# Kernel tuning notes

Hardware: AMD Instinct MI355X
Metric: run time of the kernel (lower is better)

The kernel has to match this reference:

```python
import jax, jax.numpy as jnp
import numpy as np

N = 50000        # nodes
E = 800000       # edges
D_IN = 128       # input feature dim
HID = 64         # hidden_dim
HEADS = 4
OUT = 2          # output_dim (fraud / not-fraud)
BN_EPS = 1e-5
NEG_SLOPE = 0.2  # PyG GATv2Conv default


def setup_inputs() -> dict:
    key = jax.random.key(0)
    ks = jax.random.split(key, 16)
    g = lambda k, shape, s=0.05: (jax.random.normal(k, shape, jnp.float32) * s)
    HC = HEADS * HID  # 256
    return {
        "x": jax.random.normal(ks[0], (N, D_IN), jnp.float32),
        "edge_index": jax.random.randint(ks[1], (2, E), 0, N),
        # input projection
        "W_in": g(ks[2], (D_IN, HID)), "b_in": jnp.zeros((HID,), jnp.float32),
        # GATv2 layer 0: HID -> HID, 4 heads (concat -> 256)
        "Wl0": g(ks[3], (HID, HC)), "Wr0": g(ks[4], (HID, HC)),
        "att0": g(ks[5], (HEADS, HID)), "bias0": jnp.zeros((HC,), jnp.float32),
        # GATv2 layer 1: 256 -> HID, 4 heads (concat -> 256)
        "Wl1": g(ks[6], (HC, HC)), "Wr1": g(ks[7], (HC, HC)),
        "att1": g(ks[8], (HEADS, HID)), "bias1": jnp.zeros((HC,), jnp.float32),
        # GATv2 layer 2: 256 -> OUT, 1 head
        "Wl2": g(ks[9], (HC, OUT)), "Wr2": g(ks[10], (HC, OUT)),
        "att2": g(ks[11], (1, OUT)), "bias2": jnp.zeros((OUT,), jnp.float32),
        # BatchNorm (eval mode: running stats) for the first num_layers-1 = 2 layers
        "bn_gamma": jnp.ones((2, HC), jnp.float32),
        "bn_beta": jnp.zeros((2, HC), jnp.float32),
        "bn_mean": jnp.zeros((2, HC), jnp.float32),
        "bn_var": jnp.ones((2, HC), jnp.float32),
    }


def _gatv2(h, src, dst, Wl, Wr, att, bias):
    """PyG GATv2Conv (concat=True, negative_slope=0.2). src->dst messages."""
    n = h.shape[0]
    heads, c = att.shape
    xl = (h @ Wl).reshape(n, heads, c)   # source transform
    xr = (h @ Wr).reshape(n, heads, c)   # target transform
    e = jax.nn.leaky_relu(xl[src] + xr[dst], NEG_SLOPE)       # [E, H, C]
    logits = jnp.einsum('ehc,hc->eh', e, att)                 # [E, H]
    # segment softmax over incoming edges of each destination node
    m = jax.ops.segment_max(logits, dst, num_segments=n)      # [N, H]
    ex = jnp.exp(logits - m[dst])
    denom = jax.ops.segment_sum(ex, dst, num_segments=n)
    alpha = ex / denom[dst]                                   # [E, H]
    out = jax.ops.segment_sum(xl[src] * alpha[..., None], dst, num_segments=n)
    return out.reshape(n, heads * c) + bias


def _bn_eval(h, gamma, beta, mean, var):
    return gamma * (h - mean) * jax.lax.rsqrt(var + BN_EPS) + beta


def reference(x, edge_index, W_in, b_in, Wl0, Wr0, att0, bias0,
              Wl1, Wr1, att1, bias1, Wl2, Wr2, att2, bias2,
              bn_gamma, bn_beta, bn_mean, bn_var):
    n = x.shape[0]
    loop = jnp.arange(n)
    src = jnp.concatenate([edge_index[0], loop])  # PyG add_self_loops=True
    dst = jnp.concatenate([edge_index[1], loop])

    h = jax.nn.relu(x @ W_in + b_in)              # dropout is identity in eval

    # layer 0 (no residual: 64 != 256)
    h = _gatv2(h, src, dst, Wl0, Wr0, att0, bias0)
    h = jax.nn.relu(_bn_eval(h, bn_gamma[0], bn_beta[0], bn_mean[0], bn_var[0]))

    # layer 1 (residual: 256 == 256)
    h_prev = h
    h = _gatv2(h, src, dst, Wl1, Wr1, att1, bias1)
    h = jax.nn.relu(_bn_eval(h, bn_gamma[1], bn_beta[1], bn_mean[1], bn_var[1]))
    h = h + h_prev

    # output layer, 1 head
    h = _gatv2(h, src, dst, Wl2, Wr2, att2, bias2)
    return jax.nn.log_softmax(h, axis=1)
```

## Files before the change

### kernel.cpp

```cpp
#include <hip/hip_runtime.h>
#include <hip/hip_bf16.h>
#include <math.h>


using h16     = _Float16;
using half2v  = __attribute__((ext_vector_type(2))) h16;
using half4v  = __attribute__((ext_vector_type(4))) h16;
using half8   = __attribute__((ext_vector_type(8))) h16;
using floatx2 = __attribute__((ext_vector_type(2))) float;
using floatx4 = __attribute__((ext_vector_type(4))) float;

__device__ __forceinline__ float lrelu(float x) { return x > 0.f ? x : 0.2f * x; }

__device__ __forceinline__ half2v shfl_xor_h2(half2v v, int mask) {
    float f = __builtin_bit_cast(float, v);
    f = __shfl_xor(f, mask, 64);
    return __builtin_bit_cast(half2v, f);
}

__global__ void hist_dst(const int* __restrict__ ei, int E, int* __restrict__ deg) {
    int e = blockIdx.x * blockDim.x + threadIdx.x;
    if (e < E) atomicAdd(&deg[ei[E + e]], 1);
}

__global__ __launch_bounds__(256) void scan_blk(const int* __restrict__ deg,
                                                int* __restrict__ rowstart,
                                                int* __restrict__ bsum, int N) {
    int t = blockIdx.x * 256 + threadIdx.x;
    int lane = threadIdx.x & 63, wid = threadIdx.x >> 6;
    int v = (t < N) ? ((deg[t] + 4) & ~3) : 0;
    int x = v;
#pragma unroll
    for (int off = 1; off < 64; off <<= 1) {
        int y = __shfl_up(x, off, 64);
        if (lane >= off) x += y;
    }
    __shared__ int wsum[4];
    if (lane == 63) wsum[wid] = x;
    __syncthreads();
    int add = 0;
#pragma unroll
    for (int w = 0; w < 4; ++w) if (w < wid) add += wsum[w];
    int incl = x + add;
    if (t < N) rowstart[t] = incl - v;
    if (threadIdx.x == 255) bsum[blockIdx.x] = incl;
}

__global__ __launch_bounds__(256) void scan_off(int* __restrict__ bsum, int NB) {
    int t = threadIdx.x;
    int lane = t & 63, wid = t >> 6;
    int v = (t < NB) ? bsum[t] : 0;
    int x = v;
#pragma unroll
    for (int off = 1; off < 64; off <<= 1) {
        int y = __shfl_up(x, off, 64);
        if (lane >= off) x += y;
    }
    __shared__ int wsum[4];
    if (lane == 63) wsum[wid] = x;
    __syncthreads();
    int add = 0;
#pragma unroll
    for (int w = 0; w < 4; ++w) if (w < wid) add += wsum[w];
    if (t < NB) bsum[t] = x + add - v;
}

__global__ void add_off(const int* __restrict__ bsum, const int* __restrict__ deg,
                        int* __restrict__ rowstart, int* __restrict__ cursor,
                        int* __restrict__ csr_src, int N) {
    int t = blockIdx.x * 256 + threadIdx.x;
    if (t >= N) return;
    int r = rowstart[t] + bsum[blockIdx.x];
    rowstart[t] = r;
    cursor[t] = r;
    int dg = deg[t];
    int npad = (dg + 4) & ~3;
    for (int k = dg; k < npad; ++k) csr_src[r + k] = t;
}

__global__ void scatter_src(const int* __restrict__ ei, int E,
                            int* __restrict__ cursor, int* __restrict__ csr_src) {
    int e = blockIdx.x * blockDim.x + threadIdx.x;
    if (e >= E) return;
    int d = ei[E + e];
    int pos = atomicAdd(&cursor[d], 1);
    csr_src[pos] = ei[e];
}

__device__ __forceinline__ void pack_one(const float* __restrict__ W,
                                         h16* __restrict__ Wp,
                                         int t, int K, int NC) {
    int j = t & 7;
    int l = (t >> 3) & 63;
    int rest = t >> 9;
    int NT = NC >> 4;
    int nt = rest % NT;
    int kc = rest / NT;
    int row = kc * 32 + (l >> 4) * 8 + j;
    int col = nt * 16 + (l & 15);
    Wp[t] = (h16)W[(size_t)row * NC + col];
}

__global__ void pack_all(const float* __restrict__ W_in,
                         const float* __restrict__ Wl0, const float* __restrict__ Wr0,
                         const float* __restrict__ Wl1, const float* __restrict__ Wr1,
                         h16* __restrict__ P_in,
                         h16* __restrict__ P_l0, h16* __restrict__ P_r0,
                         h16* __restrict__ P_l1, h16* __restrict__ P_r1,
                         const float4* __restrict__ x, half4v* __restrict__ xh, int n4,
                         int* __restrict__ deg, int N) {
    int t = blockIdx.x * blockDim.x + threadIdx.x;
    if (t < 8192)        pack_one(W_in, P_in, t, 128, 64);
    else if (t < 24576)  pack_one(Wl0, P_l0, t - 8192, 64, 256);
    else if (t < 40960)  pack_one(Wr0, P_r0, t - 24576, 64, 256);
    else if (t < 106496) pack_one(Wl1, P_l1, t - 40960, 256, 256);
    else if (t < 172032) pack_one(Wr1, P_r1, t - 106496, 256, 256);
    else if (t < 172032 + n4) {
        int u = t - 172032;
        float4 v = x[u];
        half4v o = { (h16)v.x, (h16)v.y, (h16)v.z, (h16)v.w };
        xh[u] = o;
    } else {
        int u = t - 172032 - n4;
        if (u < N) deg[u] = 0;
    }
}

template<int KC, int NT, bool RELU, bool DUAL>
__global__ __launch_bounds__(256) void gemm_lds(
        const h16* __restrict__ Xh,
        const h16* __restrict__ Wp0, const h16* __restrict__ Wp1,
        const float* __restrict__ bias,
        h16* __restrict__ out0, h16* __restrict__ out1, int M) {
    constexpr int K = KC * 32;
    constexpr int ldo = NT * 16;
    constexpr int CHUNK8 = NT * 64;
    constexpr int PER_THR = CHUNK8 / 256;
    __shared__ half8 wbuf[2][CHUNK8];

    const h16* Wp = (DUAL && blockIdx.y) ? Wp1 : Wp0;
    h16* outp = (DUAL && blockIdx.y) ? out1 : out0;
    const half8* WG = (const half8*)Wp;

    const int tid = threadIdx.x;
    const int wid = tid >> 6, lane = tid & 63;
    const int quad = lane >> 4, li = lane & 15;
    const int r0 = blockIdx.x * 64 + wid * 16;
    int arow = r0 + li; if (arow >= M) arow = M - 1;
    const half8* A8 = (const half8*)Xh + (size_t)arow * (K / 8) + quad;

    floatx4 acc[NT];
#pragma unroll
    for (int t = 0; t < NT; ++t) acc[t] = (floatx4){0.f, 0.f, 0.f, 0.f};

    half8 st[PER_THR];
#pragma unroll
    for (int i = 0; i < PER_THR; ++i) st[i] = WG[i * 256 + tid];
#pragma unroll
    for (int i = 0; i < PER_THR; ++i) wbuf[0][i * 256 + tid] = st[i];
    __syncthreads();

#pragma unroll
    for (int kc = 0; kc < KC; ++kc) {
        int cur = kc & 1;
        if (kc + 1 < KC) {
#pragma unroll
            for (int i = 0; i < PER_THR; ++i)
                st[i] = WG[(size_t)(kc + 1) * CHUNK8 + i * 256 + tid];
        }
        half8 a = A8[kc * 4];
#pragma unroll
        for (int nt = 0; nt < NT; ++nt) {
            half8 b = wbuf[cur][nt * 64 + lane];
            acc[nt] = __builtin_amdgcn_mfma_f32_16x16x32_f16(a, b, acc[nt], 0, 0, 0);
        }
        if (kc + 1 < KC) {
#pragma unroll
            for (int i = 0; i < PER_THR; ++i) wbuf[cur ^ 1][i * 256 + tid] = st[i];
        }
        __syncthreads();
    }

#pragma unroll
    for (int nt = 0; nt < NT; ++nt) {
#pragma unroll
        for (int reg = 0; reg < 4; ++reg) {
            int rr = r0 + quad * 4 + reg;
            if (rr >= M) continue;
            float v = acc[nt][reg];
            if (RELU) v = fmaxf(v + bias[nt * 16 + li], 0.f);
            outp[(size_t)rr * ldo + nt * 16 + li] = (h16)v;
        }
    }
}

__global__ void attn4_bn(int N, const h16* __restrict__ XL,
                         const h16* __restrict__ XR,
                         const float* __restrict__ att,
                         const int* __restrict__ rowstart, const int* __restrict__ deg,
                         const int* __restrict__ csr_src,
                         const float* __restrict__ gamma, const float* __restrict__ beta,
                         const float* __restrict__ mean, const float* __restrict__ var,
                         const float* __restrict__ bias, const h16* __restrict__ resid,
                         h16* __restrict__ outb) {
    int d = blockIdx.x * (blockDim.x >> 6) + (threadIdx.x >> 6);
    int lane = threadIdx.x & 63;
    if (d >= N) return;
    const uint2* XL64 = (const uint2*)XL;
    half4v bv = *(const half4v*)(XR + (size_t)d * 256 + lane * 4);
    float4 wf = ((const float4*)att)[lane];
    half2v b0 = bv.xy, b1 = bv.zw;
    half2v w0 = { (h16)wf.x, (h16)wf.y };
    half2v w1 = { (h16)wf.z, (h16)wf.w };
    const h16 k02 = (h16)0.2f;

    auto edge_part = [&](half4v xv) -> h16 {
        half2v e0 = xv.xy + b0, e1 = xv.zw + b1;
        half2v l0 = __builtin_elementwise_max(e0, e0 * k02);
        half2v l1 = __builtin_elementwise_max(e1, e1 * k02);
        half2v qd = l0 * w0 + l1 * w1;
        return qd.x + qd.y;
    };

    int start = rowstart[d];
    int nreal = deg[d] + 1;
    int npad  = (deg[d] + 4) & ~3;
    float l = 0.f;
    half2v acc0 = { (h16)0.f, (h16)0.f };
    half2v acc1 = { (h16)0.f, (h16)0.f };

    int4 iv = *(const int4*)(csr_src + start);
    for (int i = 0; i < npad; i += 4) {
        int4 cur = iv;
        if (i + 4 < npad) iv = *(const int4*)(csr_src + start + i + 4);
        uint2 v0 = XL64[(size_t)cur.x * 64 + lane];
        uint2 v1 = XL64[(size_t)cur.y * 64 + lane];
        uint2 v2 = XL64[(size_t)cur.z * 64 + lane];
        uint2 v3 = XL64[(size_t)cur.w * 64 + lane];
        half4v x0 = __builtin_bit_cast(half4v, v0);
        half4v x1 = __builtin_bit_cast(half4v, v1);
        half4v x2 = __builtin_bit_cast(half4v, v2);
        half4v x3 = __builtin_bit_cast(half4v, v3);
        half2v p01 = { edge_part(x0), edge_part(x1) };
        half2v p23 = { edge_part(x2), edge_part(x3) };
#pragma unroll
        for (int s = 1; s < 16; s <<= 1) {
            p01 += shfl_xor_h2(p01, s);
            p23 += shfl_xor_h2(p23, s);
        }
        int rem = nreal - i;
        float e0 = __expf((float)p01.x);
        float e1 = (rem > 1) ? __expf((float)p01.y) : 0.f;
        float e2 = (rem > 2) ? __expf((float)p23.x) : 0.f;
        float e3 = (rem > 3) ? __expf((float)p23.y) : 0.f;
        l += (e0 + e1) + (e2 + e3);
        h16 h0 = (h16)e0, h1 = (h16)e1, h2 = (h16)e2, h3 = (h16)e3;
        half2v eb0 = { h0, h0 }, eb1 = { h1, h1 }, eb2 = { h2, h2 }, eb3 = { h3, h3 };
        acc0 += eb0 * x0.xy; acc1 += eb0 * x0.zw;
        acc0 += eb1 * x1.xy; acc1 += eb1 * x1.zw;
        acc0 += eb2 * x2.xy; acc1 += eb2 * x2.zw;
        acc0 += eb3 * x3.xy; acc1 += eb3 * x3.zw;
    }
    float4 acc = { (float)acc0.x, (float)acc0.y, (float)acc1.x, (float)acc1.y };
    float inv = 1.f / l;
    float4 g  = ((const float4*)gamma)[lane];
    float4 be = ((const float4*)beta)[lane];
    float4 mu = ((const float4*)mean)[lane];
    float4 va = ((const float4*)var)[lane];
    float4 bi = ((const float4*)bias)[lane];
    float4 sc4, sh4;
    sc4.x = g.x * rsqrtf(va.x + 1e-5f); sh4.x = (bi.x - mu.x) * sc4.x + be.x;
    sc4.y = g.y * rsqrtf(va.y + 1e-5f); sh4.y = (bi.y - mu.y) * sc4.y + be.y;
    sc4.z = g.z * rsqrtf(va.z + 1e-5f); sh4.z = (bi.z - mu.z) * sc4.z + be.z;
    sc4.w = g.w * rsqrtf(va.w + 1e-5f); sh4.w = (bi.w - mu.w) * sc4.w + be.w;
    float4 o;
    o.x = fmaxf(acc.x * inv * sc4.x + sh4.x, 0.f);
    o.y = fmaxf(acc.y * inv * sc4.y + sh4.y, 0.f);
    o.z = fmaxf(acc.z * inv * sc4.z + sh4.z, 0.f);
    o.w = fmaxf(acc.w * inv * sc4.w + sh4.w, 0.f);
    if (resid) {
        half4v rv = *(const half4v*)(resid + (size_t)d * 256 + lane * 4);
        o.x += (float)rv.x; o.y += (float)rv.y;
        o.z += (float)rv.z; o.w += (float)rv.w;
    }
    half4v ob = { (h16)o.x, (h16)o.y, (h16)o.z, (h16)o.w };
    *(half4v*)(outb + (size_t)d * 256 + lane * 4) = ob;
}

__global__ void gemm2_wave(const h16* __restrict__ X, const float* __restrict__ Wl,
                           const float* __restrict__ Wr, float* __restrict__ xl2,
                           float* __restrict__ xr2, int N) {
    int t = blockIdx.x * blockDim.x + threadIdx.x;
    int n = t >> 4;
    int sl = t & 15;
    if (n >= N) return;
    const half4v* Xr = (const half4v*)(X + (size_t)n * 256);
    const float4* Wl4 = (const float4*)Wl;
    const float4* Wr4 = (const float4*)Wr;
    float l0 = 0.f, l1 = 0.f, r0 = 0.f, r1 = 0.f;
#pragma unroll
    for (int j = 0; j < 4; ++j) {
        int idx = sl + j * 16;
        half4v xh = Xr[idx];
        float4 xv = { (float)xh.x, (float)xh.y, (float)xh.z, (float)xh.w };
        float4 wa = Wl4[idx * 2];
        float4 wb = Wl4[idx * 2 + 1];
        l0 += xv.x * wa.x + xv.y * wa.z + xv.z * wb.x + xv.w * wb.z;
        l1 += xv.x * wa.y + xv.y * wa.w + xv.z * wb.y + xv.w * wb.w;
        wa = Wr4[idx * 2]; wb = Wr4[idx * 2 + 1];
        r0 += xv.x * wa.x + xv.y * wa.z + xv.z * wb.x + xv.w * wb.z;
        r1 += xv.x * wa.y + xv.y * wa.w + xv.z * wb.y + xv.w * wb.w;
    }
#pragma unroll
    for (int off = 1; off < 16; off <<= 1) {
        l0 += __shfl_xor(l0, off, 64);
        l1 += __shfl_xor(l1, off, 64);
        r0 += __shfl_xor(r0, off, 64);
        r1 += __shfl_xor(r1, off, 64);
    }
    if (sl == 0) {
        xl2[n * 2] = l0; xl2[n * 2 + 1] = l1;
        xr2[n * 2] = r0; xr2[n * 2 + 1] = r1;
    }
}

__global__ void attn1_16(int N, const float* __restrict__ xl2, const float* __restrict__ xr2,
                         const float* __restrict__ att, const float* __restrict__ bias,
                         const int* __restrict__ rowstart, const int* __restrict__ deg,
                         const int* __restrict__ csr_src, float* __restrict__ out) {
    int t = blockIdx.x * blockDim.x + threadIdx.x;
    int d = t >> 4, sl = t & 15;
    if (d >= N) return;
    float a0 = att[0], a1 = att[1];
    float2 xr = ((const float2*)xr2)[d];
    float b0 = xr.x, b1 = xr.y;
    int st = rowstart[d];
    int nreal = deg[d] + 1;
    int npad  = (deg[d] + 4) & ~3;
    float l = 0.f, ac0 = 0.f, ac1 = 0.f;
    for (int i = sl; i < npad; i += 16) {
        int s = csr_src[st + i];
        float2 xv = ((const float2*)xl2)[s];
        float q = lrelu(xv.x + b0) * a0 + lrelu(xv.y + b1) * a1;
        float e = (i < nreal) ? __expf(q) : 0.f;
        l += e; ac0 += e * xv.x; ac1 += e * xv.y;
    }
#pragma unroll
    for (int off = 1; off < 16; off <<= 1) {
        l   += __shfl_xor(l, off, 64);
        ac0 += __shfl_xor(ac0, off, 64);
        ac1 += __shfl_xor(ac1, off, 64);
    }
    if (sl == 0) {
        float inv = 1.f / l;
        float v0 = ac0 * inv + bias[0];
        float v1 = ac1 * inv + bias[1];
        float mx = fmaxf(v0, v1);
        float lse = mx + logf(__expf(v0 - mx) + __expf(v1 - mx));
        out[d * 2] = v0 - lse;
        out[d * 2 + 1] = v1 - lse;
    }
}

extern "C" void kernel_launch(void* const* d_in, const int* in_sizes, int n_in,
                              void* d_out, int out_size, void* d_ws, size_t ws_size,
                              hipStream_t stream) {
    const float* x        = (const float*)d_in[0];
    const int*   ei       = (const int*)  d_in[1];
    const float* W_in     = (const float*)d_in[2];
    const float* b_in     = (const float*)d_in[3];
    const float* Wl0      = (const float*)d_in[4];
    const float* Wr0      = (const float*)d_in[5];
    const float* att0     = (const float*)d_in[6];
    const float* bias0    = (const float*)d_in[7];
    const float* Wl1      = (const float*)d_in[8];
    const float* Wr1      = (const float*)d_in[9];
    const float* att1     = (const float*)d_in[10];
    const float* bias1    = (const float*)d_in[11];
    const float* Wl2      = (const float*)d_in[12];
    const float* Wr2      = (const float*)d_in[13];
    const float* att2     = (const float*)d_in[14];
    const float* bias2    = (const float*)d_in[15];
    const float* bn_gamma = (const float*)d_in[16];
    const float* bn_beta  = (const float*)d_in[17];
    const float* bn_mean  = (const float*)d_in[18];
    const float* bn_var   = (const float*)d_in[19];

    const int N  = in_sizes[0] / 128;
    const int E  = in_sizes[1] / 2;
    const int NB = (N + 255) / 256;

    float* ws = (float*)d_ws;
    size_t off = 0;
    float* XL2  = ws + off; off += (size_t)N * 2;
    float* XR2  = ws + off; off += (size_t)N * 2;
    h16* Ah   = (h16*)(ws + off); off += (size_t)N * 128;
    h16* Bh   = (h16*)(ws + off); off += (size_t)N * 128;
    h16* Ch   = (h16*)(ws + off); off += (size_t)N * 128;
    h16* Dh   = (h16*)(ws + off); off += (size_t)N * 128;
    h16* H0h  = (h16*)(ws + off); off += (size_t)N * 32;
    h16* xh   = (h16*)(ws + off); off += (size_t)N * 64;
    h16* Wp_in = (h16*)(ws + off); off += 4096;
    h16* Wp_l0 = (h16*)(ws + off); off += 8192;
    h16* Wp_r0 = (h16*)(ws + off); off += 8192;
    h16* Wp_l1 = (h16*)(ws + off); off += 32768;
    h16* Wp_r1 = (h16*)(ws + off); off += 32768;
    int* ip = (int*)(ws + off);
    int* deg      = ip;              ip += N;
    int* rowstart = ip;              ip += N;
    int* cursor   = ip;              ip += N;
    int* bsum     = ip;              ip += NB;
    int* csr_src  = ip;              ip += E + 4 * N + 64;

    const int PACK_T = 172032 + N * 32 + N;
    pack_all<<<(PACK_T + 255) / 256, 256, 0, stream>>>(
        W_in, Wl0, Wr0, Wl1, Wr1, Wp_in, Wp_l0, Wp_r0, Wp_l1, Wp_r1,
        (const float4*)x, (half4v*)xh, N * 32, deg, N);

    hist_dst<<<(E + 255) / 256, 256, 0, stream>>>(ei, E, deg);
    scan_blk<<<NB, 256, 0, stream>>>(deg, rowstart, bsum, N);
    scan_off<<<1, 256, 0, stream>>>(bsum, NB);
    add_off<<<NB, 256, 0, stream>>>(bsum, deg, rowstart, cursor, csr_src, N);
    scatter_src<<<(E + 255) / 256, 256, 0, stream>>>(ei, E, cursor, csr_src);

    const int GBM = (N + 63) / 64;

    gemm_lds<4, 4, true, false><<<GBM, 256, 0, stream>>>(
        xh, Wp_in, nullptr, b_in, H0h, nullptr, N);

    gemm_lds<2, 16, false, true><<<dim3(GBM, 2), 256, 0, stream>>>(
        H0h, Wp_l0, Wp_r0, nullptr, Ah, Bh, N);
    attn4_bn<<<(N + 3) / 4, 256, 0, stream>>>(N, Ah, Bh, att0, rowstart, deg, csr_src,
                                              bn_gamma, bn_beta, bn_mean, bn_var,
                                              bias0, nullptr, Ch);

    gemm_lds<8, 16, false, true><<<dim3(GBM, 2), 256, 0, stream>>>(
        Ch, Wp_l1, Wp_r1, nullptr, Ah, Bh, N);
    attn4_bn<<<(N + 3) / 4, 256, 0, stream>>>(N, Ah, Bh, att1, rowstart, deg, csr_src,
                                              bn_gamma + 256, bn_beta + 256, bn_mean + 256,
                                              bn_var + 256, bias1, Ch, Dh);

    gemm2_wave<<<(N * 16 + 255) / 256, 256, 0, stream>>>(Dh, Wl2, Wr2, XL2, XR2, N);
    attn1_16<<<(N * 16 + 255) / 256, 256, 0, stream>>>(N, XL2, XR2, att2, bias2,
                                                       rowstart, deg, csr_src, (float*)d_out);
}
```

Before: 415.9 us.

## Process two destination nodes per wave in GATv2 attention with 16-byte gathers

The attention+BN kernel now assigns two destination nodes per 64-lane wave, with each half-wave of 32 lanes handling 8 fp16 features per lane via 16-byte gathers instead of 8-byte ones. The per-head reduction shrinks to 3 shuffle steps. Both halves loop to the larger padded degree, clamping index prefetch and masking extra edges. The aim is fewer waves, wider memory transactions and fewer shuffles per edge, at the cost of divergence when the two nodes have unequal degrees and more registers per lane.

```diff
diff --git a/kernel.cpp b/kernel.cpp
--- a/kernel.cpp
+++ b/kernel.cpp
@@ -203,88 +203,124 @@
                          const float* __restrict__ mean, const float* __restrict__ var,
                          const float* __restrict__ bias, const h16* __restrict__ resid,
                          h16* __restrict__ outb) {
-    int d = blockIdx.x * (blockDim.x >> 6) + (threadIdx.x >> 6);
+    int wv = blockIdx.x * (blockDim.x >> 6) + (threadIdx.x >> 6);
+    int d0 = wv * 2;
+    if (d0 >= N) return;
     int lane = threadIdx.x & 63;
-    if (d >= N) return;
-    const uint2* XL64 = (const uint2*)XL;
-    half4v bv = *(const half4v*)(XR + (size_t)d * 256 + lane * 4);
-    float4 wf = ((const float4*)att)[lane];
-    half2v b0 = bv.xy, b1 = bv.zw;
-    half2v w0 = { (h16)wf.x, (h16)wf.y };
-    half2v w1 = { (h16)wf.z, (h16)wf.w };
+    int sl   = lane & 31;
+    int dh   = d0 + (lane >> 5);
+    bool dvalid = dh < N;
+    int dr = dvalid ? dh : d0;
+
+    int start = rowstart[dr];
+    int dg    = deg[dr];
+    int nreal = dg + 1;
+    int npad  = (dg + 4) & ~3;
+    int npmax = max(npad, __shfl_xor(npad, 32, 64));
+
+    union H8 { uint4 u; half2v h[4]; };
+    H8 bv, wt;
+    bv.u = *(const uint4*)(XR + (size_t)dr * 256 + sl * 8);
+    {
+        const float* ar = att + (sl >> 3) * 64 + (sl & 7) * 8;
+        float4 wa = *(const float4*)ar;
+        float4 wb = *(const float4*)(ar + 4);
+        wt.h[0] = half2v{(h16)wa.x, (h16)wa.y};
+        wt.h[1] = half2v{(h16)wa.z, (h16)wa.w};
+        wt.h[2] = half2v{(h16)wb.x, (h16)wb.y};
+        wt.h[3] = half2v{(h16)wb.z, (h16)wb.w};
+    }
     const h16 k02 = (h16)0.2f;
-
-    auto edge_part = [&](half4v xv) -> h16 {
-        half2v e0 = xv.xy + b0, e1 = xv.zw + b1;
-        half2v l0 = __builtin_elementwise_max(e0, e0 * k02);
-        half2v l1 = __builtin_elementwise_max(e1, e1 * k02);
-        half2v qd = l0 * w0 + l1 * w1;
-        return qd.x + qd.y;
+    const uint4* XLv = (const uint4*)XL;
+
+    auto ep = [&](const H8& x) -> h16 {
+        half2v q = half2v{(h16)0, (h16)0};
+#pragma unroll
+        for (int j = 0; j < 4; ++j) {
+            half2v e  = x.h[j] + bv.h[j];
+            half2v lr = __builtin_elementwise_max(e, e * k02);
+            q += lr * wt.h[j];
+        }
+        return q.x + q.y;
     };
 
-    int start = rowstart[d];
-    int nreal = deg[d] + 1;
-    int npad  = (deg[d] + 4) & ~3;
     float l = 0.f;
-    half2v acc0 = { (h16)0.f, (h16)0.f };
-    half2v acc1 = { (h16)0.f, (h16)0.f };
+    half2v acc[4] = {half2v{(h16)0,(h16)0}, half2v{(h16)0,(h16)0},
+                     half2v{(h16)0,(h16)0}, half2v{(h16)0,(h16)0}};
 
     int4 iv = *(const int4*)(csr_src + start);
-    for (int i = 0; i < npad; i += 4) {
+    for (int i = 0; i < npmax; i += 4) {
         int4 cur = iv;
-        if (i + 4 < npad) iv = *(const int4*)(csr_src + start + i + 4);
-        uint2 v0 = XL64[(size_t)cur.x * 64 + lane];
-        uint2 v1 = XL64[(size_t)cur.y * 64 + lane];
-        uint2 v2 = XL64[(size_t)cur.z * 64 + lane];
-        uint2 v3 = XL64[(size_t)cur.w * 64 + lane];
-        half4v x0 = __builtin_bit_cast(half4v, v0);
-        half4v x1 = __builtin_bit_cast(half4v, v1);
-        half4v x2 = __builtin_bit_cast(half4v, v2);
-        half4v x3 = __builtin_bit_cast(half4v, v3);
-        half2v p01 = { edge_part(x0), edge_part(x1) };
-        half2v p23 = { edge_part(x2), edge_part(x3) };
-#pragma unroll
-        for (int s = 1; s < 16; s <<= 1) {
+        if (i + 4 < npmax) {
+            int nxt = min(i + 4, npad - 4);
+            iv = *(const int4*)(csr_src + start + nxt);
+        }
+        H8 x0, x1, x2, x3;
+        x0.u = XLv[(size_t)(unsigned)cur.x * 32 + sl];
+        x1.u = XLv[(size_t)(unsigned)cur.y * 32 + sl];
+        x2.u = XLv[(size_t)(unsigned)cur.z * 32 + sl];
+        x3.u = XLv[(size_t)(unsigned)cur.w * 32 + sl];
+        half2v p01 = { ep(x0), ep(x1) };
+        half2v p23 = { ep(x2), ep(x3) };
+#pragma unroll
+        for (int s = 1; s < 8; s <<= 1) {
             p01 += shfl_xor_h2(p01, s);
             p23 += shfl_xor_h2(p23, s);
         }
         int rem = nreal - i;
-        float e0 = __expf((float)p01.x);
+        float e0 = (rem > 0) ? __expf((float)p01.x) : 0.f;
         float e1 = (rem > 1) ? __expf((float)p01.y) : 0.f;
         float e2 = (rem > 2) ? __expf((float)p23.x) : 0.f;
         float e3 = (rem > 3) ? __expf((float)p23.y) : 0.f;
         l += (e0 + e1) + (e2 + e3);
         h16 h0 = (h16)e0, h1 = (h16)e1, h2 = (h16)e2, h3 = (h16)e3;
-        half2v eb0 = { h0, h0 }, eb1 = { h1, h1 }, eb2 = { h2, h2 }, eb3 = { h3, h3 };
-        acc0 += eb0 * x0.xy; acc1 += eb0 * x0.zw;
-        acc0 += eb1 * x1.xy; acc1 += eb1 * x1.zw;
-        acc0 += eb2 * x2.xy; acc1 += eb2 * x2.zw;
-        acc0 += eb3 * x3.xy; acc1 += eb3 * x3.zw;
-    }
-    float4 acc = { (float)acc0.x, (float)acc0.y, (float)acc1.x, (float)acc1.y };
+        half2v eb0 = {h0,h0}, eb1 = {h1,h1}, eb2 = {h2,h2}, eb3 = {h3,h3};
+#pragma unroll
+        for (int j = 0; j < 4; ++j) {
+            acc[j] += eb0 * x0.h[j];
+            acc[j] += eb1 * x1.h[j];
+            acc[j] += eb2 * x2.h[j];
+            acc[j] += eb3 * x3.h[j];
+        }
+    }
+
     float inv = 1.f / l;
-    float4 g  = ((const float4*)gamma)[lane];
-    float4 be = ((const float4*)beta)[lane];
-    float4 mu = ((const float4*)mean)[lane];
-    float4 va = ((const float4*)var)[lane];
-    float4 bi = ((const float4*)bias)[lane];
-    float4 sc4, sh4;
-    sc4.x = g.x * rsqrtf(va.x + 1e-5f); sh4.x = (bi.x - mu.x) * sc4.x + be.x;
-    sc4.y = g.y * rsqrtf(va.y + 1e-5f); sh4.y = (bi.y - mu.y) * sc4.y + be.y;
-    sc4.z = g.z * rsqrtf(va.z + 1e-5f); sh4.z = (bi.z - mu.z) * sc4.z + be.z;
-    sc4.w = g.w * rsqrtf(va.w + 1e-5f); sh4.w = (bi.w - mu.w) * sc4.w + be.w;
-    float4 o;
-    o.x = fmaxf(acc.x * inv * sc4.x + sh4.x, 0.f);
-    o.y = fmaxf(acc.y * inv * sc4.y + sh4.y, 0.f);
-    o.z = fmaxf(acc.z * inv * sc4.z + sh4.z, 0.f);
-    o.w = fmaxf(acc.w * inv * sc4.w + sh4.w, 0.f);
+    float oc[8];
+#pragma unroll
+    for (int j = 0; j < 4; ++j) { oc[2*j] = (float)acc[j].x; oc[2*j+1] = (float)acc[j].y; }
+    const float4* g4  = (const float4*)gamma;
+    const float4* be4 = (const float4*)beta;
+    const float4* mu4 = (const float4*)mean;
+    const float4* va4 = (const float4*)var;
+    const float4* bi4 = (const float4*)bias;
+    float o[8];
+#pragma unroll
+    for (int q = 0; q < 2; ++q) {
+        float4 g  = g4[sl*2+q],  bb = be4[sl*2+q], mu = mu4[sl*2+q];
+        float4 va = va4[sl*2+q], bi = bi4[sl*2+q];
+        float s0 = g.x * rsqrtf(va.x + 1e-5f);
+        float s1 = g.y * rsqrtf(va.y + 1e-5f);
+        float s2 = g.z * rsqrtf(va.z + 1e-5f);
+        float s3 = g.w * rsqrtf(va.w + 1e-5f);
+        o[q*4+0] = fmaxf(oc[q*4+0]*inv*s0 + (bi.x-mu.x)*s0 + bb.x, 0.f);
+        o[q*4+1] = fmaxf(oc[q*4+1]*inv*s1 + (bi.y-mu.y)*s1 + bb.y, 0.f);
+        o[q*4+2] = fmaxf(oc[q*4+2]*inv*s2 + (bi.z-mu.z)*s2 + bb.z, 0.f);
+        o[q*4+3] = fmaxf(oc[q*4+3]*inv*s3 + (bi.w-mu.w)*s3 + bb.w, 0.f);
+    }
     if (resid) {
-        half4v rv = *(const half4v*)(resid + (size_t)d * 256 + lane * 4);
-        o.x += (float)rv.x; o.y += (float)rv.y;
-        o.z += (float)rv.z; o.w += (float)rv.w;
-    }
-    half4v ob = { (h16)o.x, (h16)o.y, (h16)o.z, (h16)o.w };
-    *(half4v*)(outb + (size_t)d * 256 + lane * 4) = ob;
+        H8 rv; rv.u = *(const uint4*)(resid + (size_t)dr * 256 + sl * 8);
+#pragma unroll
+        for (int j = 0; j < 4; ++j) {
+            o[2*j]   += (float)rv.h[j].x;
+            o[2*j+1] += (float)rv.h[j].y;
+        }
+    }
+    if (dvalid) {
+        H8 ov;
+#pragma unroll
+        for (int j = 0; j < 4; ++j) ov.h[j] = half2v{(h16)o[2*j], (h16)o[2*j+1]};
+        *(uint4*)(outb + (size_t)dh * 256 + sl * 8) = ov.u;
+    }
 }
 
 __global__ void gemm2_wave(const h16* __restrict__ X, const float* __restrict__ Wl,
@@ -430,13 +466,13 @@
 
     gemm_lds<2, 16, false, true><<<dim3(GBM, 2), 256, 0, stream>>>(
         H0h, Wp_l0, Wp_r0, nullptr, Ah, Bh, N);
-    attn4_bn<<<(N + 3) / 4, 256, 0, stream>>>(N, Ah, Bh, att0, rowstart, deg, csr_src,
+    attn4_bn<<<(N + 7) / 8, 256, 0, stream>>>(N, Ah, Bh, att0, rowstart, deg, csr_src,
                                               bn_gamma, bn_beta, bn_mean, bn_var,
                                               bias0, nullptr, Ch);
 
     gemm_lds<8, 16, false, true><<<dim3(GBM, 2), 256, 0, stream>>>(
         Ch, Wp_l1, Wp_r1, nullptr, Ah, Bh, N);
-    attn4_bn<<<(N + 3) / 4, 256, 0, stream>>>(N, Ah, Bh, att1, rowstart, deg, csr_src,
+    attn4_bn<<<(N + 7) / 8, 256, 0, stream>>>(N, Ah, Bh, att1, rowstart, deg, csr_src,
                                               bn_gamma + 256, bn_beta + 256, bn_mean + 256,
                                               bn_var + 256, bias1, Ch, Dh);
 
```

Result: faster. 405.4 us (-2.5%).
